# Kernel tuning notes

Hardware: AMD Instinct MI355X
Metric: run time of the kernel (lower is better)

The kernel has to match this reference:

```python
import jax, jax.numpy as jnp
import numpy as np

D_MODEL = 1024
NUM_HEADS = 16
HEAD_DIM = D_MODEL // NUM_HEADS
B, T = 2, 2048


def setup_inputs() -> dict:
    key = jax.random.key(0)
    kx, kq, kk, kv, ko = jax.random.split(key, 5)
    s = 1.0 / np.sqrt(D_MODEL)  # ~Linear init scale
    return {
        "x": jax.random.normal(kx, (B, T, D_MODEL), dtype=jnp.float32),
        "Wq": jax.random.normal(kq, (D_MODEL, D_MODEL), dtype=jnp.float32) * s,
        "Wk": jax.random.normal(kk, (D_MODEL, D_MODEL), dtype=jnp.float32) * s,
        "Wv": jax.random.normal(kv, (D_MODEL, D_MODEL), dtype=jnp.float32) * s,
        "Wo": jax.random.normal(ko, (D_MODEL, D_MODEL), dtype=jnp.float32) * s,
    }


def reference(x, Wq, Wk, Wv, Wo):
    Bc, Tc, _ = x.shape
    H, D = NUM_HEADS, HEAD_DIM
    scale = jnp.sqrt(jnp.asarray(D, x.dtype))
    # torch Linear (bias=False): y = x @ W^T
    q = (x @ Wq.T).reshape(Bc, Tc, H, D).transpose(0, 2, 1, 3)  # [B,H,T,D]
    k = (x @ Wk.T).reshape(Bc, Tc, H, D).transpose(0, 2, 1, 3)
    v = (x @ Wv.T).reshape(Bc, Tc, H, D).transpose(0, 2, 1, 3)
    scores = jnp.einsum("bhtd,bhsd->bhts", q, k) / scale  # [B,H,T,T]
    # causal bias: upper triangle (strictly future positions) gets -1e9
    causal_bias = jnp.triu(jnp.ones((Tc, Tc), dtype=jnp.float32), k=1) * -1e9
    scores = scores + causal_bias
    weights = jax.nn.softmax(scores, axis=-1)
    # dropout is identity in eval / p=0
    out = jnp.einsum("bhts,bhsd->bhtd", weights, v)  # [B,H,T,D]
    out = out.transpose(0, 2, 1, 3).reshape(Bc, Tc, H * D)
    return out @ Wo.T
```

## Files before the change

kernel.cpp:

```cpp
#include <hip/hip_runtime.h>
#include <hip/hip_bf16.h>

typedef __bf16 bf16_t;
typedef __bf16 bf16x2 __attribute__((ext_vector_type(2)));
typedef __bf16 bf16x4 __attribute__((ext_vector_type(4)));
typedef __bf16 bf16x8 __attribute__((ext_vector_type(8)));
typedef float  f32x4  __attribute__((ext_vector_type(4)));

#define D_MODEL 1024
#define HEADS   16
#define HD      64
#define BB      2
#define TT      2048
#define MROWS   (BB*TT)

#define GLDS16(g, l) __builtin_amdgcn_global_load_lds( \
    (const __attribute__((address_space(1))) void*)(g), \
    (__attribute__((address_space(3))) void*)(l), 16, 0, 0)

static __device__ __forceinline__ int pack_bf16(float a, float b) {
    bf16x2 t; t[0] = (bf16_t)a; t[1] = (bf16_t)b;
    return __builtin_bit_cast(int, t);
}

__global__ __launch_bounds__(256) void cvt_all_kernel(const float* __restrict__ x,
                                                      const float* __restrict__ wq,
                                                      const float* __restrict__ wk,
                                                      const float* __restrict__ wv,
                                                      const float* __restrict__ wo,
                                                      bf16_t* __restrict__ dst) {
    const int i = blockIdx.x * 256 + threadIdx.x;
    const float* src;
    int s;
    if (i < 1048576) { src = x; s = i; }
    else {
        int j = i - 1048576;
        int w = j >> 18;
        s = j & 262143;
        src = (w == 0) ? wq : (w == 1) ? wk : (w == 2) ? wv : wo;
    }
    float4 v = reinterpret_cast<const float4*>(src)[s];
    bf16x4 o;
    o[0] = (bf16_t)v.x; o[1] = (bf16_t)v.y; o[2] = (bf16_t)v.z; o[3] = (bf16_t)v.w;
    reinterpret_cast<bf16x4*>(dst)[i] = o;
}

template<int MODE, int BN>
__global__ __launch_bounds__(256) void gemm_bt(const bf16_t* __restrict__ A,
                                               const bf16_t* __restrict__ Bw,
                                               void* __restrict__ Cout,
                                               int M, int N, int K) {
    constexpr int NI = BN / 32;
    __shared__ __align__(16) bf16_t As[128*32];
    __shared__ __align__(16) bf16_t Bs[BN*32];
    const int tid   = threadIdx.x;
    const int lane  = tid & 63;
    const int wave  = tid >> 6;
    const int col16 = lane & 15;
    const int quad  = lane >> 4;
    const int wrow  = (wave & 1) * 64;
    const int wcol  = (wave >> 1) * (BN / 2);
    const int bm    = blockIdx.y * 128;
    const int bn    = blockIdx.x * BN;

    const int lr = tid >> 2;
    const int lc = (tid & 3) * 8;

    const bf16_t* agp = &A [(size_t)(bm + lr)*K + lc];
    const bf16_t* bgp = &Bw[(size_t)(bn + lr)*K + lc];
    const size_t half = (size_t)64 * K;
    bf16_t* as_lo = &As[wave*512];
    bf16_t* as_hi = &As[2048 + wave*512];
    bf16_t* bs_lo = &Bs[wave*512];
    bf16_t* bs_hi = &Bs[2048 + wave*512];

    f32x4 acc[4][NI];
#pragma unroll
    for (int i = 0; i < 4; i++)
#pragma unroll
        for (int j = 0; j < NI; j++) acc[i][j] = (f32x4){0.f, 0.f, 0.f, 0.f};

    for (int k0 = 0; k0 < K; k0 += 32) {
        GLDS16(agp + k0,        as_lo);
        GLDS16(agp + half + k0, as_hi);
        GLDS16(bgp + k0,        bs_lo);
        if (BN == 128) GLDS16(bgp + half + k0, bs_hi);
        __syncthreads();

        bf16x8 af[4], bfr[NI];
#pragma unroll
        for (int mi = 0; mi < 4; mi++)
            af[mi] = *reinterpret_cast<const bf16x8*>(&As[(wrow + mi*16 + col16)*32 + quad*8]);
#pragma unroll
        for (int ni = 0; ni < NI; ni++)
            bfr[ni] = *reinterpret_cast<const bf16x8*>(&Bs[(wcol + ni*16 + col16)*32 + quad*8]);
#pragma unroll
        for (int mi = 0; mi < 4; mi++)
#pragma unroll
            for (int ni = 0; ni < NI; ni++)
                acc[mi][ni] = __builtin_amdgcn_mfma_f32_16x16x32_bf16(af[mi], bfr[ni], acc[mi][ni], 0, 0, 0);
        __syncthreads();
    }

#pragma unroll
    for (int mi = 0; mi < 4; mi++) {
#pragma unroll
        for (int r = 0; r < 4; r++) {
            const int gm = bm + wrow + mi*16 + quad*4 + r;
            const int t  = gm & (TT - 1);
            const int b  = gm >> 11;
#pragma unroll
            for (int ni = 0; ni < NI; ni++) {
                const int gn = bn + wcol + ni*16 + col16;
                float v = acc[mi][ni][r];
                if (MODE == 2) {
                    reinterpret_cast<float*>(Cout)[(size_t)gm * N + gn] = v;
                } else {
                    const int which = gn >> 10;
                    if (which == 0) v *= 0.18033688f;
                    const int n = gn & 1023;
                    const int h = n >> 6, d = n & 63;
                    const size_t off = (size_t)(which == 2 ? 3 : which) * MROWS * D_MODEL;
                    bf16_t* base = reinterpret_cast<bf16_t*>(Cout) + off;
                    base[(((size_t)(b*HEADS + h))*TT + t)*HD + d] = (bf16_t)v;
                }
            }
        }
    }
}

__global__ __launch_bounds__(256) void transpose_v(const bf16_t* __restrict__ V,
                                                   bf16_t* __restrict__ Vt) {
    __shared__ bf16_t tile[64][72];
    const int tid = threadIdx.x;
    const int bh = blockIdx.y;
    const int t0 = blockIdx.x * 64;
    const bf16_t* src = V + ((size_t)bh * TT + t0) * HD;
#pragma unroll
    for (int i = 0; i < 2; i++) {
        const int r = i*32 + (tid >> 3), c = (tid & 7) * 8;
        *reinterpret_cast<bf16x8*>(&tile[r][c]) =
            *reinterpret_cast<const bf16x8*>(&src[(size_t)r * HD + c]);
    }
    __syncthreads();
    bf16_t* dst = Vt + (size_t)bh * HD * TT + t0;
#pragma unroll
    for (int i = 0; i < 2; i++) {
        const int d = i*32 + (tid >> 3), tc = (tid & 7) * 8;
        bf16x8 o;
#pragma unroll
        for (int j = 0; j < 8; j++) o[j] = tile[tc + j][d];
        *reinterpret_cast<bf16x8*>(&dst[(size_t)d * TT + tc]) = o;
    }
}

__global__ __launch_bounds__(256, 5) void attn_kernel(const bf16_t* __restrict__ Q,
                                                      const bf16_t* __restrict__ Kk,
                                                      const bf16_t* __restrict__ Vt,
                                                      bf16_t* __restrict__ O) {
    __shared__ __align__(16) bf16_t Ks[2][64*64];
    __shared__ __align__(16) bf16_t Vs[2][64*64];

    const int tid   = threadIdx.x;
    const int lane  = tid & 63;
    const int wave  = tid >> 6;
    const int col16 = lane & 15;
    const int quad  = lane >> 4;

    const int bx = blockIdx.x;
    const int r_ = bx >> 8, s_ = bx & 255;
    const int bh = s_ & 31;
    const int qt = (r_ == 0) ? (24 + (s_ >> 5))
                             : ((r_ - 1) * 8 + 7 - (s_ >> 5));
    const int qb    = qt * 64;
    const int qbase = qb + wave * 16;
    const int nkt   = qt + 1;

    const bf16_t* Qb = Q  + (size_t)bh * TT * HD;
    const bf16_t* Kb = Kk + (size_t)bh * TT * HD;
    const bf16_t* Vb = Vt + (size_t)bh * HD * TT;

    bf16x8 qf0 = *reinterpret_cast<const bf16x8*>(&Qb[(size_t)(qbase + col16)*HD + quad*8]);
    bf16x8 qf1 = *reinterpret_cast<const bf16x8*>(&Qb[(size_t)(qbase + col16)*HD + 32 + quad*8]);

    const int srow = (tid >> 3) & 31;
    const int sg   = ((lane & 7) ^ (srow & 7)) * 8;

    auto stage = [&](int kt, int buf) {
        const int s0 = kt * 64;
        GLDS16(&Kb[(size_t)(s0 + srow)*HD + sg],        &Ks[buf][wave*512]);
        GLDS16(&Kb[(size_t)(s0 + srow + 32)*HD + sg],   &Ks[buf][2048 + wave*512]);
        GLDS16(&Vb[(size_t)srow*TT + s0 + sg],          &Vs[buf][wave*512]);
        GLDS16(&Vb[(size_t)(srow + 32)*TT + s0 + sg],   &Vs[buf][2048 + wave*512]);
    };

    f32x4 acc[4];
#pragma unroll
    for (int i = 0; i < 4; i++) acc[i] = (f32x4){0.f,0.f,0.f,0.f};
    float lsum = 0.f;

    const int x7 = col16 & 7;
    const int a1 = ((quad & 1) * 32 + col16) * 4;
    const int a2 = a1 + 64;
    const bool hi = quad >= 2;

    stage(0, 0);
    __syncthreads();

    for (int kt = 0; kt < nkt; kt++) {
        const int buf = kt & 1;
        if (kt + 1 < nkt) stage(kt + 1, buf ^ 1);
        const int s0 = kt * 64;
        const bool diag = (kt == nkt - 1);

        int pk[4][2];
#pragma unroll
        for (int c = 0; c < 4; c++) {
            bf16x8 k0 = *reinterpret_cast<const bf16x8*>(
                &Ks[buf][(c*16 + col16)*64 + ((0*4 + quad) ^ x7)*8]);
            bf16x8 k1 = *reinterpret_cast<const bf16x8*>(
                &Ks[buf][(c*16 + col16)*64 + ((1*4 + quad) ^ x7)*8]);
            f32x4 sv = __builtin_amdgcn_mfma_f32_16x16x32_bf16(k0, qf0, (f32x4){0.f,0.f,0.f,0.f}, 0, 0, 0);
            sv       = __builtin_amdgcn_mfma_f32_16x16x32_bf16(k1, qf1, sv, 0, 0, 0);

            float pr[4];
#pragma unroll
            for (int r = 0; r < 4; r++) pr[r] = exp2f(sv[r]);
            if (diag) {
#pragma unroll
                for (int r = 0; r < 4; r++)
                    if (s0 + c*16 + quad*4 + r > qbase + col16) pr[r] = 0.f;
            }
            lsum += (pr[0] + pr[1]) + (pr[2] + pr[3]);
            pk[c][0] = pack_bf16(pr[0], pr[1]);
            pk[c][1] = pack_bf16(pr[2], pr[3]);
        }

#pragma unroll
        for (int kc = 0; kc < 2; kc++) {
            int b0l = __builtin_amdgcn_ds_bpermute(a1, pk[2*kc][0]);
            int b0h = __builtin_amdgcn_ds_bpermute(a1, pk[2*kc+1][0]);
            int b1l = __builtin_amdgcn_ds_bpermute(a1, pk[2*kc][1]);
            int b1h = __builtin_amdgcn_ds_bpermute(a1, pk[2*kc+1][1]);
            int b2l = __builtin_amdgcn_ds_bpermute(a2, pk[2*kc][0]);
            int b2h = __builtin_amdgcn_ds_bpermute(a2, pk[2*kc+1][0]);
            int b3l = __builtin_amdgcn_ds_bpermute(a2, pk[2*kc][1]);
            int b3h = __builtin_amdgcn_ds_bpermute(a2, pk[2*kc+1][1]);
            int4 bi = { hi ? b0h : b0l, hi ? b1h : b1l, hi ? b2h : b2l, hi ? b3h : b3l };
            bf16x8 pf = __builtin_bit_cast(bf16x8, bi);
#pragma unroll
            for (int c = 0; c < 4; c++) {
                bf16x8 vf = *reinterpret_cast<const bf16x8*>(
                    &Vs[buf][(c*16 + col16)*64 + ((kc*4 + quad) ^ x7)*8]);
                acc[c] = __builtin_amdgcn_mfma_f32_16x16x32_bf16(vf, pf, acc[c], 0, 0, 0);
            }
        }
        __syncthreads();
    }

    float l = lsum;
    l += __shfl_xor(l, 16);
    l += __shfl_xor(l, 32);
    const float inv = 1.0f / l;

    const int b_ = bh >> 4, h = bh & 15;
    const int t = qbase + col16;
    bf16_t* Ob = &O[(((size_t)(b_*TT + t))*HEADS + h)*HD + quad*4];
#pragma unroll
    for (int c = 0; c < 4; c++) {
        bf16x4 o4;
#pragma unroll
        for (int r = 0; r < 4; r++) o4[r] = (bf16_t)(acc[c][r] * inv);
        *reinterpret_cast<bf16x4*>(&Ob[c*16]) = o4;
    }
}

extern "C" void kernel_launch(void* const* d_in, const int* in_sizes, int n_in,
                              void* d_out, int out_size, void* d_ws, size_t ws_size,
                              hipStream_t stream) {
    const float* x  = (const float*)d_in[0];
    const float* Wq = (const float*)d_in[1];
    const float* Wk = (const float*)d_in[2];
    const float* Wv = (const float*)d_in[3];
    const float* Wo = (const float*)d_in[4];
    float* out = (float*)d_out;

    bf16_t* Xb  = (bf16_t*)d_ws;
    bf16_t* Wqb = Xb  + (size_t)MROWS * D_MODEL;
    bf16_t* Wob = Wqb + (size_t)3 * D_MODEL * D_MODEL;
    bf16_t* Qw  = Wob + (size_t)D_MODEL * D_MODEL;
    bf16_t* Kw  = Qw  + (size_t)MROWS * D_MODEL;
    bf16_t* Vt  = Kw  + (size_t)MROWS * D_MODEL;
    bf16_t* Ow  = Vt  + (size_t)MROWS * D_MODEL;

    cvt_all_kernel<<<(MROWS*D_MODEL + 4*D_MODEL*D_MODEL) / 4 / 256, 256, 0, stream>>>(
        x, Wq, Wk, Wv, Wo, Xb);

    dim3 gqkv(3 * D_MODEL / 128, MROWS / 128);
    gemm_bt<0,128><<<gqkv, 256, 0, stream>>>(Xb, Wqb, Qw, MROWS, 3 * D_MODEL, D_MODEL);

    dim3 gt(TT / 64, BB * HEADS);
    transpose_v<<<gt, 256, 0, stream>>>(Ow, Vt);

    attn_kernel<<<dim3(1024), 256, 0, stream>>>(Qw, Kw, Vt, Ow);

    dim3 go(D_MODEL / 64, MROWS / 128);
    gemm_bt<2,64><<<go, 256, 0, stream>>>(Ow, Wob, out, MROWS, D_MODEL, D_MODEL);
}
```

Before: 191.0 us.

## Split long causal query tiles across two blocks and merge partial outputs

Query tiles 16-31, which have the longest causal key ranges, are each split into two halves of the key range processed by separate blocks. The halves write unnormalized partial outputs and row sums to scratch (reusing the Xb workspace region), and a new combine kernel sums them and normalizes. The aim is to cut tail imbalance in the attention grid at the cost of an extra kernel launch, extra global traffic and bf16 rounding of the partial sums. Merging by plain addition relies on exp2 without a running max, as in the existing kernel.

```diff
diff --git a/kernel.cpp b/kernel.cpp
--- a/kernel.cpp
+++ b/kernel.cpp
@@ -157,7 +157,9 @@
 __global__ __launch_bounds__(256, 5) void attn_kernel(const bf16_t* __restrict__ Q,
                                                       const bf16_t* __restrict__ Kk,
                                                       const bf16_t* __restrict__ Vt,
-                                                      bf16_t* __restrict__ O) {
+                                                      bf16_t* __restrict__ O,
+                                                      bf16_t* __restrict__ Opart,
+                                                      float* __restrict__ Lpart) {
     __shared__ __align__(16) bf16_t Ks[2][64*64];
     __shared__ __align__(16) bf16_t Vs[2][64*64];
 
@@ -168,13 +170,29 @@
     const int quad  = lane >> 4;
 
     const int bx = blockIdx.x;
-    const int r_ = bx >> 8, s_ = bx & 255;
-    const int bh = s_ & 31;
-    const int qt = (r_ == 0) ? (24 + (s_ >> 5))
-                             : ((r_ - 1) * 8 + 7 - (s_ >> 5));
+    int bh, qt, kbeg, kend, half_ = 0, pairId = 0;
+    bool split;
+    if (bx < 1024) {
+        split = true;
+        bh = bx & 31;
+        const int p  = bx >> 5;
+        half_ = p & 1;
+        const int pp = p >> 1;
+        qt = (pp < 8) ? (31 - pp) : (8 + pp);
+        const int m = (qt + 2) >> 1;
+        kbeg = half_ ? m : 0;
+        kend = half_ ? (qt + 1) : m;
+        pairId = (qt - 16) * 32 + bh;
+    } else {
+        split = false;
+        const int j = bx - 1024;
+        bh = j & 31;
+        const int p = j >> 5;
+        qt = (p < 8) ? (15 - p) : (p - 8);
+        kbeg = 0; kend = qt + 1;
+    }
     const int qb    = qt * 64;
     const int qbase = qb + wave * 16;
-    const int nkt   = qt + 1;
 
     const bf16_t* Qb = Q  + (size_t)bh * TT * HD;
     const bf16_t* Kb = Kk + (size_t)bh * TT * HD;
@@ -204,14 +222,14 @@
     const int a2 = a1 + 64;
     const bool hi = quad >= 2;
 
-    stage(0, 0);
+    stage(kbeg, 0);
     __syncthreads();
 
-    for (int kt = 0; kt < nkt; kt++) {
-        const int buf = kt & 1;
-        if (kt + 1 < nkt) stage(kt + 1, buf ^ 1);
+    for (int kt = kbeg; kt < kend; kt++) {
+        const int buf = (kt - kbeg) & 1;
+        if (kt + 1 < kend) stage(kt + 1, buf ^ 1);
         const int s0 = kt * 64;
-        const bool diag = (kt == nkt - 1);
+        const bool diag = (kt == qt);
 
         int pk[4][2];
 #pragma unroll
@@ -261,18 +279,53 @@
     float l = lsum;
     l += __shfl_xor(l, 16);
     l += __shfl_xor(l, 32);
-    const float inv = 1.0f / l;
-
+
+    if (split) {
+        const int qloc = wave*16 + col16;
+        if (quad == 0) Lpart[(pairId*2 + half_)*64 + qloc] = l;
+        bf16_t* Pb = &Opart[(((size_t)(pairId*2 + half_))*64 + qloc)*64 + quad*4];
+#pragma unroll
+        for (int c = 0; c < 4; c++) {
+            bf16x4 o4;
+#pragma unroll
+            for (int r = 0; r < 4; r++) o4[r] = (bf16_t)acc[c][r];
+            *reinterpret_cast<bf16x4*>(&Pb[c*16]) = o4;
+        }
+    } else {
+        const float inv = 1.0f / l;
+        const int b_ = bh >> 4, h = bh & 15;
+        const int t = qbase + col16;
+        bf16_t* Ob = &O[(((size_t)(b_*TT + t))*HEADS + h)*HD + quad*4];
+#pragma unroll
+        for (int c = 0; c < 4; c++) {
+            bf16x4 o4;
+#pragma unroll
+            for (int r = 0; r < 4; r++) o4[r] = (bf16_t)(acc[c][r] * inv);
+            *reinterpret_cast<bf16x4*>(&Ob[c*16]) = o4;
+        }
+    }
+}
+
+__global__ __launch_bounds__(256) void combine_kernel(const bf16_t* __restrict__ Opart,
+                                                      const float* __restrict__ Lpart,
+                                                      bf16_t* __restrict__ O) {
+    const int idx = blockIdx.x * 256 + threadIdx.x;
+    const int d8 = (idx & 7) * 8;
+    const int q  = (idx >> 3) & 63;
+    const int pr = idx >> 9;
+    const int qt = 16 + (pr >> 5);
+    const int bh = pr & 31;
+    const float la = Lpart[(pr*2    )*64 + q];
+    const float lb = Lpart[(pr*2 + 1)*64 + q];
+    const float inv = 1.0f / (la + lb);
+    bf16x8 a = *reinterpret_cast<const bf16x8*>(&Opart[(((size_t)(pr*2    ))*64 + q)*64 + d8]);
+    bf16x8 b = *reinterpret_cast<const bf16x8*>(&Opart[(((size_t)(pr*2 + 1))*64 + q)*64 + d8]);
+    bf16x8 o;
+#pragma unroll
+    for (int i = 0; i < 8; i++) o[i] = (bf16_t)(((float)a[i] + (float)b[i]) * inv);
     const int b_ = bh >> 4, h = bh & 15;
-    const int t = qbase + col16;
-    bf16_t* Ob = &O[(((size_t)(b_*TT + t))*HEADS + h)*HD + quad*4];
-#pragma unroll
-    for (int c = 0; c < 4; c++) {
-        bf16x4 o4;
-#pragma unroll
-        for (int r = 0; r < 4; r++) o4[r] = (bf16_t)(acc[c][r] * inv);
-        *reinterpret_cast<bf16x4*>(&Ob[c*16]) = o4;
-    }
+    const int t = qt*64 + q;
+    *reinterpret_cast<bf16x8*>(&O[(((size_t)(b_*TT + t))*HEADS + h)*HD + d8]) = o;
 }
 
 extern "C" void kernel_launch(void* const* d_in, const int* in_sizes, int n_in,
@@ -292,6 +345,8 @@
     bf16_t* Kw  = Qw  + (size_t)MROWS * D_MODEL;
     bf16_t* Vt  = Kw  + (size_t)MROWS * D_MODEL;
     bf16_t* Ow  = Vt  + (size_t)MROWS * D_MODEL;
+    bf16_t* Opart = (bf16_t*)d_ws;
+    float*  Lpart = (float*)((char*)d_ws + (size_t)8*1024*1024);
 
     cvt_all_kernel<<<(MROWS*D_MODEL + 4*D_MODEL*D_MODEL) / 4 / 256, 256, 0, stream>>>(
         x, Wq, Wk, Wv, Wo, Xb);
@@ -302,7 +357,9 @@
     dim3 gt(TT / 64, BB * HEADS);
     transpose_v<<<gt, 256, 0, stream>>>(Ow, Vt);
 
-    attn_kernel<<<dim3(1024), 256, 0, stream>>>(Qw, Kw, Vt, Ow);
+    attn_kernel<<<dim3(1536), 256, 0, stream>>>(Qw, Kw, Vt, Ow, Opart, Lpart);
+
+    combine_kernel<<<dim3(1024), 256, 0, stream>>>(Opart, Lpart, Ow);
 
     dim3 go(D_MODEL / 64, MROWS / 128);
     gemm_bt<2,64><<<go, 256, 0, stream>>>(Ow, Wob, out, MROWS, D_MODEL, D_MODEL);
```

Result: slower. 202.4 us (+5.9%).
